# Kernel optimization log

Hardware: AMD Instinct MI355X
Metric: run time of the kernel (lower is better)

The kernel has to match this reference:

```python
import jax, jax.numpy as jnp
from jax import lax
import numpy as np

B, T, V, H = 512, 512, 96, 128


def setup_inputs() -> dict:
    key = jax.random.key(0)
    ks = jax.random.split(key, 8)
    # one-hot character inputs [B, T, V]
    idx = jax.random.randint(ks[0], (B, T), 0, V)
    x = jax.nn.one_hot(idx, V, dtype=jnp.float32)
    s_ih = 1.0 / np.sqrt(H)  # PyTorch nn.RNN init: U(-1/sqrt(H), 1/sqrt(H))
    W_ih = jax.random.uniform(ks[1], (H, V), jnp.float32, -s_ih, s_ih)
    b_ih = jax.random.uniform(ks[2], (H,), jnp.float32, -s_ih, s_ih)
    W_hh = jax.random.uniform(ks[3], (H, H), jnp.float32, -s_ih, s_ih)
    b_hh = jax.random.uniform(ks[4], (H,), jnp.float32, -s_ih, s_ih)
    s_fc = 1.0 / np.sqrt(H)
    W_fc = jax.random.uniform(ks[5], (V, H), jnp.float32, -s_fc, s_fc)
    b_fc = jax.random.uniform(ks[6], (V,), jnp.float32, -s_fc, s_fc)
    return {"x": x, "W_ih": W_ih, "b_ih": b_ih, "W_hh": W_hh,
            "b_hh": b_hh, "W_fc": W_fc, "b_fc": b_fc}


def reference(x, W_ih, b_ih, W_hh, b_hh, W_fc, b_fc):
    # Precompute input projection for all timesteps (batched GEMM):
    # for one-hot x this is effectively an embedding row gather.
    xW = jnp.einsum('btv,hv->bth', x, W_ih) + b_ih  # [B, T, H]

    def step(h, xt):  # h: [B, H], xt: [B, H]
        h_new = jnp.tanh(xt + h @ W_hh.T + b_hh)
        return h_new, None

    h0 = jnp.zeros((x.shape[0], W_hh.shape[0]), x.dtype)
    hT, _ = lax.scan(step, h0, jnp.swapaxes(xW, 0, 1))  # scan over T
    # fc on the last hidden state only
    return hT @ W_fc.T + b_fc  # [B, V]
```

## Files before the change

kernel.cpp:

```cpp
#include <hip/hip_runtime.h>

#define B_ 512
#define T_ 512
#define V_ 96
#define H_ 128
#define XST 132
#define K2F 2.8853900817779268f

typedef _Float16 half8 __attribute__((ext_vector_type(8)));
typedef float    f32x4 __attribute__((ext_vector_type(4)));

__global__ __launch_bounds__(256) void onehot_idx_kernel(
    const float4* __restrict__ x4, int n4, int* __restrict__ idx)
{
    int stride = gridDim.x * blockDim.x;
    for (int e4 = blockIdx.x * blockDim.x + threadIdx.x; e4 < n4; e4 += stride) {
        float4 v = x4[e4];
        int base = e4 * 4;
        if (v.x > 0.5f) idx[(base + 0) / V_] = (base + 0) % V_;
        if (v.y > 0.5f) idx[(base + 1) / V_] = (base + 1) % V_;
        if (v.z > 0.5f) idx[(base + 2) / V_] = (base + 2) % V_;
        if (v.w > 0.5f) idx[(base + 3) / V_] = (base + 3) % V_;
    }
}

__global__ __launch_bounds__(256) void build_xwg_kernel(
    const float* __restrict__ W_ih, const float* __restrict__ b_ih,
    const float* __restrict__ b_hh, float* __restrict__ xwg)
{
    int e = blockIdx.x * 256 + threadIdx.x;
    if (e < V_ * H_) {
        int v = e >> 7, up = e & 127;
        int u = (up & 7) * 16 + (up >> 3);
        xwg[e] = (W_ih[u * V_ + v] + b_ih[u] + b_hh[u]) * K2F;
    }
}

__global__ __launch_bounds__(256) void build_wB_kernel(
    const float* __restrict__ W_hh, _Float16* __restrict__ wB)
{
    int e = blockIdx.x * 256 + threadIdx.x;
    if (e < 16384) {
        int reg = e & 7, lane = (e >> 3) & 63, nt = (e >> 9) & 7, ks = e >> 12;
        int unit = ks * 32 + (lane >> 4) * 8 + reg;
        int n    = nt * 16 + (lane & 15);
        wB[e] = (_Float16)(K2F * W_hh[n * H_ + unit]);
    }
}

__global__ __launch_bounds__(256) void build_wBfc_kernel(
    const float* __restrict__ W_fc, _Float16* __restrict__ wBfc)
{
    int e = blockIdx.x * 256 + threadIdx.x;
    if (e < 12288) {
        int reg = e & 7, lane = (e >> 3) & 63;
        int nt = (e >> 9) % 6, ks = e / 3072;
        int unit = ks * 32 + (lane >> 4) * 8 + reg;
        int n    = nt * 16 + (lane & 15);
        wBfc[e] = (_Float16)W_fc[n * H_ + unit];
    }
}

__global__ __launch_bounds__(256, 1) void rnn_mfma4_kernel(
    const uint4* __restrict__ wBg, const uint4* __restrict__ wBfcg,
    const float* __restrict__ xwg, const int* __restrict__ idx,
    const float* __restrict__ b_fc, float* __restrict__ out)
{
    const int bb  = blockIdx.x;
    const int tid = threadIdx.x;
    const int w   = tid >> 6;
    const int l   = tid & 63;
    const int lo  = l & 15, g = l >> 4;

    __shared__ float         xwl[V_ * XST];
    __shared__ _Float16      hs[2][16][136];
    __shared__ unsigned char idxT[T_ * 16];

    for (int e = tid; e < V_ * H_; e += 256) {
        int v = e >> 7, up = e & 127;
        xwl[v * XST + up] = xwg[e];
    }
    for (int e = tid; e < 16 * T_; e += 256) {
        int row = e >> 9, t = e & 511;
        idxT[t * 16 + row] = (unsigned char)idx[(bb * 16 + row) * T_ + t];
    }
    for (int e = tid; e < 16 * 136; e += 256)
        hs[0][e / 136][e % 136] = (_Float16)0.f;

    uint4 wb[4][2];
    #pragma unroll
    for (int ks = 0; ks < 4; ++ks)
        #pragma unroll
        for (int q = 0; q < 2; ++q)
            wb[ks][q] = wBg[(ks * 8 + 2 * w + q) * 64 + l];

    __syncthreads();

    int cur = 0;
    #pragma clang loop unroll(disable)
    for (int t = 0; t < T_; ++t) {
        unsigned idw;
        __builtin_memcpy(&idw, &idxT[t * 16 + 4 * g], 4);

        half8 aF[4];
        #pragma unroll
        for (int ks = 0; ks < 4; ++ks)
            __builtin_memcpy(&aF[ks], &hs[cur][lo][ks * 32 + g * 8], 16);

        float2 xwc[4];
        #pragma unroll
        for (int j = 0; j < 4; ++j) {
            int id = (idw >> (8 * j)) & 255;
            __builtin_memcpy(&xwc[j], &xwl[id * XST + lo * 8 + 2 * w], 8);
        }

        f32x4 p0 = {0.f,0.f,0.f,0.f}, p1 = {0.f,0.f,0.f,0.f};
        f32x4 q0 = {0.f,0.f,0.f,0.f}, q1 = {0.f,0.f,0.f,0.f};
        #pragma unroll
        for (int ks = 0; ks < 2; ++ks) {
            union { uint4 u; half8 h; } u0, u1, u2, u3;
            u0.u = wb[ks][0];     u1.u = wb[ks][1];
            u2.u = wb[ks + 2][0]; u3.u = wb[ks + 2][1];
            p0 = __builtin_amdgcn_mfma_f32_16x16x32_f16(aF[ks],     u0.h, p0, 0, 0, 0);
            p1 = __builtin_amdgcn_mfma_f32_16x16x32_f16(aF[ks],     u1.h, p1, 0, 0, 0);
            q0 = __builtin_amdgcn_mfma_f32_16x16x32_f16(aF[ks + 2], u2.h, q0, 0, 0, 0);
            q1 = __builtin_amdgcn_mfma_f32_16x16x32_f16(aF[ks + 2], u3.h, q1, 0, 0, 0);
        }
        f32x4 acc0 = p0 + q0, acc1 = p1 + q1;

        #pragma unroll
        for (int j = 0; j < 4; ++j) {
            float E0 = __builtin_amdgcn_exp2f(acc0[j] + xwc[j].x);
            float E1 = __builtin_amdgcn_exp2f(acc1[j] + xwc[j].y);
            float h0 = 1.0f - 2.0f * __builtin_amdgcn_rcpf(E0 + 1.0f);
            float h1 = 1.0f - 2.0f * __builtin_amdgcn_rcpf(E1 + 1.0f);
            hs[cur ^ 1][4 * g + j][(2 * w + 0) * 16 + lo] = (_Float16)h0;
            hs[cur ^ 1][4 * g + j][(2 * w + 1) * 16 + lo] = (_Float16)h1;
        }
        cur ^= 1;
        __syncthreads();
    }

    half8 aE[4];
    #pragma unroll
    for (int ks = 0; ks < 4; ++ks)
        __builtin_memcpy(&aE[ks], &hs[cur][lo][ks * 32 + g * 8], 16);
    #pragma unroll
    for (int q = 0; q < 2; ++q) {
        const int NT = 2 * w + q;
        if (NT < 6) {
            float bf = b_fc[NT * 16 + lo];
            f32x4 acc = {bf, bf, bf, bf};
            #pragma unroll
            for (int ks = 0; ks < 4; ++ks) {
                union { uint4 u; half8 h; } ub;
                ub.u = wBfcg[(ks * 6 + NT) * 64 + l];
                acc = __builtin_amdgcn_mfma_f32_16x16x32_f16(aE[ks], ub.h, acc, 0, 0, 0);
            }
            #pragma unroll
            for (int j = 0; j < 4; ++j)
                out[(bb * 16 + 4 * g + j) * V_ + NT * 16 + lo] = acc[j];
        }
    }
}

extern "C" void kernel_launch(void* const* d_in, const int* in_sizes, int n_in,
                              void* d_out, int out_size, void* d_ws, size_t ws_size,
                              hipStream_t stream)
{
    const float* x    = (const float*)d_in[0];
    const float* W_ih = (const float*)d_in[1];
    const float* b_ih = (const float*)d_in[2];
    const float* W_hh = (const float*)d_in[3];
    const float* b_hh = (const float*)d_in[4];
    const float* W_fc = (const float*)d_in[5];
    const float* b_fc = (const float*)d_in[6];
    float* out = (float*)d_out;

    char* ws = (char*)d_ws;
    int*      idx  = (int*)ws;
    float*    xwg  = (float*)(ws + (size_t)B_ * T_ * 4);
    _Float16* wB   = (_Float16*)((char*)xwg + V_ * H_ * 4);
    _Float16* wBfc = (_Float16*)((char*)wB + 16384 * 2);

    const int n4 = (B_ * T_ * V_) / 4;
    hipLaunchKernelGGL(onehot_idx_kernel, dim3(2048), dim3(256), 0, stream,
                       (const float4*)x, n4, idx);
    hipLaunchKernelGGL(build_xwg_kernel, dim3((V_ * H_ + 255) / 256), dim3(256),
                       0, stream, W_ih, b_ih, b_hh, xwg);
    hipLaunchKernelGGL(build_wB_kernel, dim3(64), dim3(256), 0, stream, W_hh, wB);
    hipLaunchKernelGGL(build_wBfc_kernel, dim3(48), dim3(256), 0, stream, W_fc, wBfc);
    hipLaunchKernelGGL(rnn_mfma4_kernel, dim3(B_ / 16), dim3(256), 0, stream,
                       (const uint4*)wB, (const uint4*)wBfc, xwg, idx, b_fc, out);
}
```

Baseline: 224.9 us.

## Transpose MFMA operands so hidden-state outputs are written as contiguous vectors

Swaps the MFMA A/B roles so that weights become the A operand and the hidden state the B operand, producing transposed accumulators (hidden unit by batch row). Each lane now writes four consecutive fp16 hidden values per tile with one 8-byte store instead of scattered 2-byte stores. The input projection is loaded as vectors and used as the accumulator initial value, which removes the per-element adds. Permutations in the precompute kernels are adjusted to match. The cost is a different LDS access pattern that may bring bank conflicts, plus per-lane index reads.

```diff
diff --git a/kernel.cpp b/kernel.cpp
--- a/kernel.cpp
+++ b/kernel.cpp
@@ -30,8 +30,7 @@
 {
     int e = blockIdx.x * 256 + threadIdx.x;
     if (e < V_ * H_) {
-        int v = e >> 7, up = e & 127;
-        int u = (up & 7) * 16 + (up >> 3);
+        int v = e >> 7, u = e & 127;
         xwg[e] = (W_ih[u * V_ + v] + b_ih[u] + b_hh[u]) * K2F;
     }
 }
@@ -41,10 +40,10 @@
 {
     int e = blockIdx.x * 256 + threadIdx.x;
     if (e < 16384) {
-        int reg = e & 7, lane = (e >> 3) & 63, nt = (e >> 9) & 7, ks = e >> 12;
-        int unit = ks * 32 + (lane >> 4) * 8 + reg;
-        int n    = nt * 16 + (lane & 15);
-        wB[e] = (_Float16)(K2F * W_hh[n * H_ + unit]);
+        int reg = e & 7, lane = (e >> 3) & 63, mt = (e >> 9) & 7, ks = e >> 12;
+        int kin = ks * 32 + (lane >> 4) * 8 + reg;
+        int m   = mt * 16 + (lane & 15);
+        wB[e] = (_Float16)(K2F * W_hh[m * H_ + kin]);
     }
 }
 
@@ -54,10 +53,10 @@
     int e = blockIdx.x * 256 + threadIdx.x;
     if (e < 12288) {
         int reg = e & 7, lane = (e >> 3) & 63;
-        int nt = (e >> 9) % 6, ks = e / 3072;
-        int unit = ks * 32 + (lane >> 4) * 8 + reg;
-        int n    = nt * 16 + (lane & 15);
-        wBfc[e] = (_Float16)W_fc[n * H_ + unit];
+        int mt = (e >> 9) % 6, ks = e / 3072;
+        int kin = ks * 32 + (lane >> 4) * 8 + reg;
+        int m   = mt * 16 + (lane & 15);
+        wBfc[e] = (_Float16)W_fc[m * H_ + kin];
     }
 }
 
@@ -77,8 +76,8 @@
     __shared__ unsigned char idxT[T_ * 16];
 
     for (int e = tid; e < V_ * H_; e += 256) {
-        int v = e >> 7, up = e & 127;
-        xwl[v * XST + up] = xwg[e];
+        int v = e >> 7, u = e & 127;
+        xwl[v * XST + u] = xwg[e];
     }
     for (int e = tid; e < 16 * T_; e += 256) {
         int row = e >> 9, t = e & 511;
@@ -87,79 +86,74 @@
     for (int e = tid; e < 16 * 136; e += 256)
         hs[0][e / 136][e % 136] = (_Float16)0.f;
 
-    uint4 wb[4][2];
+    uint4 wa[4][2];
     #pragma unroll
     for (int ks = 0; ks < 4; ++ks)
         #pragma unroll
         for (int q = 0; q < 2; ++q)
-            wb[ks][q] = wBg[(ks * 8 + 2 * w + q) * 64 + l];
+            wa[ks][q] = wBg[(ks * 8 + 2 * w + q) * 64 + l];
 
     __syncthreads();
 
     int cur = 0;
     #pragma clang loop unroll(disable)
     for (int t = 0; t < T_; ++t) {
-        unsigned idw;
-        __builtin_memcpy(&idw, &idxT[t * 16 + 4 * g], 4);
+        const int id = idxT[t * 16 + lo];
 
-        half8 aF[4];
+        f32x4 xw0, xw1;
+        __builtin_memcpy(&xw0, &xwl[id * XST + 32 * w + 4 * g], 16);
+        __builtin_memcpy(&xw1, &xwl[id * XST + 32 * w + 16 + 4 * g], 16);
+
+        half8 bF[4];
         #pragma unroll
         for (int ks = 0; ks < 4; ++ks)
-            __builtin_memcpy(&aF[ks], &hs[cur][lo][ks * 32 + g * 8], 16);
+            __builtin_memcpy(&bF[ks], &hs[cur][lo][ks * 32 + g * 8], 16);
 
-        float2 xwc[4];
-        #pragma unroll
-        for (int j = 0; j < 4; ++j) {
-            int id = (idw >> (8 * j)) & 255;
-            __builtin_memcpy(&xwc[j], &xwl[id * XST + lo * 8 + 2 * w], 8);
-        }
-
-        f32x4 p0 = {0.f,0.f,0.f,0.f}, p1 = {0.f,0.f,0.f,0.f};
-        f32x4 q0 = {0.f,0.f,0.f,0.f}, q1 = {0.f,0.f,0.f,0.f};
+        f32x4 p0 = xw0, p1 = xw1;
+        f32x4 q0 = {0.f, 0.f, 0.f, 0.f}, q1 = {0.f, 0.f, 0.f, 0.f};
         #pragma unroll
         for (int ks = 0; ks < 2; ++ks) {
             union { uint4 u; half8 h; } u0, u1, u2, u3;
-            u0.u = wb[ks][0];     u1.u = wb[ks][1];
-            u2.u = wb[ks + 2][0]; u3.u = wb[ks + 2][1];
-            p0 = __builtin_amdgcn_mfma_f32_16x16x32_f16(aF[ks],     u0.h, p0, 0, 0, 0);
-            p1 = __builtin_amdgcn_mfma_f32_16x16x32_f16(aF[ks],     u1.h, p1, 0, 0, 0);
-            q0 = __builtin_amdgcn_mfma_f32_16x16x32_f16(aF[ks + 2], u2.h, q0, 0, 0, 0);
-            q1 = __builtin_amdgcn_mfma_f32_16x16x32_f16(aF[ks + 2], u3.h, q1, 0, 0, 0);
+            u0.u = wa[ks][0];     u1.u = wa[ks][1];
+            u2.u = wa[ks + 2][0]; u3.u = wa[ks + 2][1];
+            p0 = __builtin_amdgcn_mfma_f32_16x16x32_f16(u0.h, bF[ks],     p0, 0, 0, 0);
+            p1 = __builtin_amdgcn_mfma_f32_16x16x32_f16(u1.h, bF[ks],     p1, 0, 0, 0);
+            q0 = __builtin_amdgcn_mfma_f32_16x16x32_f16(u2.h, bF[ks + 2], q0, 0, 0, 0);
+            q1 = __builtin_amdgcn_mfma_f32_16x16x32_f16(u3.h, bF[ks + 2], q1, 0, 0, 0);
         }
         f32x4 acc0 = p0 + q0, acc1 = p1 + q1;
 
+        _Float16 o0[4], o1[4];
         #pragma unroll
         for (int j = 0; j < 4; ++j) {
-            float E0 = __builtin_amdgcn_exp2f(acc0[j] + xwc[j].x);
-            float E1 = __builtin_amdgcn_exp2f(acc1[j] + xwc[j].y);
-            float h0 = 1.0f - 2.0f * __builtin_amdgcn_rcpf(E0 + 1.0f);
-            float h1 = 1.0f - 2.0f * __builtin_amdgcn_rcpf(E1 + 1.0f);
-            hs[cur ^ 1][4 * g + j][(2 * w + 0) * 16 + lo] = (_Float16)h0;
-            hs[cur ^ 1][4 * g + j][(2 * w + 1) * 16 + lo] = (_Float16)h1;
+            float E0 = __builtin_amdgcn_exp2f(acc0[j]);
+            float E1 = __builtin_amdgcn_exp2f(acc1[j]);
+            o0[j] = (_Float16)(1.0f - 2.0f * __builtin_amdgcn_rcpf(E0 + 1.0f));
+            o1[j] = (_Float16)(1.0f - 2.0f * __builtin_amdgcn_rcpf(E1 + 1.0f));
         }
+        __builtin_memcpy(&hs[cur ^ 1][lo][32 * w + 4 * g], o0, 8);
+        __builtin_memcpy(&hs[cur ^ 1][lo][32 * w + 16 + 4 * g], o1, 8);
         cur ^= 1;
         __syncthreads();
     }
 
-    half8 aE[4];
+    half8 bE[4];
     #pragma unroll
     for (int ks = 0; ks < 4; ++ks)
-        __builtin_memcpy(&aE[ks], &hs[cur][lo][ks * 32 + g * 8], 16);
+        __builtin_memcpy(&bE[ks], &hs[cur][lo][ks * 32 + g * 8], 16);
     #pragma unroll
     for (int q = 0; q < 2; ++q) {
-        const int NT = 2 * w + q;
-        if (NT < 6) {
-            float bf = b_fc[NT * 16 + lo];
-            f32x4 acc = {bf, bf, bf, bf};
+        const int MT = 2 * w + q;
+        if (MT < 6) {
+            f32x4 acc;
+            __builtin_memcpy(&acc, &b_fc[MT * 16 + 4 * g], 16);
             #pragma unroll
             for (int ks = 0; ks < 4; ++ks) {
-                union { uint4 u; half8 h; } ub;
-                ub.u = wBfcg[(ks * 6 + NT) * 64 + l];
-                acc = __builtin_amdgcn_mfma_f32_16x16x32_f16(aE[ks], ub.h, acc, 0, 0, 0);
+                union { uint4 u; half8 h; } ua;
+                ua.u = wBfcg[(ks * 6 + MT) * 64 + l];
+                acc = __builtin_amdgcn_mfma_f32_16x16x32_f16(ua.h, bE[ks], acc, 0, 0, 0);
             }
-            #pragma unroll
-            for (int j = 0; j < 4; ++j)
-                out[(bb * 16 + 4 * g + j) * V_ + NT * 16 + lo] = acc[j];
+            __builtin_memcpy(&out[(bb * 16 + lo) * V_ + MT * 16 + 4 * g], &acc, 16);
         }
     }
 }
```

Result: faster. 198.0 us (-11.9%).
